# Kernel tuning notes

Measured on AMD Instinct MI355X. Metric: run time of the kernel, lower is better.

Reference implementation:

```python
import jax, jax.numpy as jnp
import numpy as np

B, D = 65536, 784          # batch, input features
H = 256                     # delegator feature (hidden) dim
L = 64                      # num_leaves (experts)
C = 10                      # num_classes


def setup_inputs() -> dict:
    key = jax.random.key(0)
    ks = jax.random.split(key, 7)
    s_in = 1.0 / np.sqrt(D)
    s_h = 1.0 / np.sqrt(H)
    return {
        "x": jax.random.normal(ks[0], (B, D), dtype=jnp.float32),
        "Wf": jax.random.normal(ks[1], (D, H), dtype=jnp.float32) * s_in,   # Node feature proj
        "bf": jnp.zeros((H,), dtype=jnp.float32),
        "Wr": jax.random.normal(ks[2], (D, L), dtype=jnp.float32) * s_in,   # Node router proj
        "br": jnp.zeros((L,), dtype=jnp.float32),
        "Wl": jax.random.normal(ks[3], (L, H, C), dtype=jnp.float32) * s_h,  # per-leaf linear
        "bl": jnp.zeros((L, C), dtype=jnp.float32),
    }


def reference(x, Wf, bf, Wr, br, Wl, bl):
    # Delegator (Node): features + routing probabilities
    features = jax.nn.relu(x @ Wf + bf)                 # [B, H]
    probs = jax.nn.softmax(x @ Wr + br, axis=1)         # [B, L]
    choices = jnp.argmax(probs, axis=1)                 # [B] top-1 leaf per sample
    # Per-sample leaf dispatch: gather each sample's leaf weights, then a
    # batched vec-mat product (memory-bound gather, low FLOP/byte).
    Wc = Wl[choices]                                    # [B, H, C]
    bc = bl[choices]                                    # [B, C]
    predictions = jnp.einsum("bh,bhc->bc", features, Wc) + bc  # [B, C]
    return predictions
```

## Files before the change

### kernel.cpp

```cpp
#include <hip/hip_runtime.h>
#include <stdint.h>

#define B_ROWS 65536
#define D_IN   784
#define H_DIM  256
#define L_LEAF 64
#define C_CLS  10
#define NSTEP2 25
#define BTILE2 20480
#define GAP_THRESH 0.03f

using f32x4    = __attribute__((ext_vector_type(4))) float;
using bf16x8   = __attribute__((ext_vector_type(8))) short;
using ushort8v = __attribute__((ext_vector_type(8))) unsigned short;
using ushort4v = __attribute__((ext_vector_type(4))) unsigned short;

#define O_FLAGCNT  0
#define O_CHOICES  4096
#define O_FLAGROWS (O_CHOICES + B_ROWS * 4)
#define O_WT       (O_FLAGROWS + B_ROWS * 4)
#define WT_BYTES   (NSTEP2 * BTILE2)
#define O_FEAT     (O_WT + WT_BYTES)
#define O_WLB      (O_FEAT + (size_t)B_ROWS * H_DIM * 2)
#define WS_BASE    O_WLB
#define WS_FULL    (O_WLB + (size_t)L_LEAF * H_DIM * C_CLS * 2)

__device__ __forceinline__ unsigned short f2bf(float f) {
    union { float f; unsigned int u; } c; c.f = f;
    unsigned int u = c.u;
    return (unsigned short)((u + 0x7fffu + ((u >> 16) & 1u)) >> 16);
}
__device__ __forceinline__ float bf2f(unsigned short u) {
    union { unsigned int u; float f; } c; c.u = ((unsigned int)u) << 16;
    return c.f;
}
__device__ __forceinline__ unsigned int cvtpk(float a, float b) {
    unsigned int r;
    asm("v_cvt_pk_bf16_f32 %0, %1, %2" : "=v"(r) : "v"(a), "v"(b));
    return r;
}

__device__ __forceinline__ void gload_lds16(const void* g, void* l) {
    __builtin_amdgcn_global_load_lds(
        (const __attribute__((address_space(1))) unsigned int*)g,
        (__attribute__((address_space(3))) unsigned int*)l, 16, 0, 0);
}

__global__ void k0_prep(const float* __restrict__ Wf, const float* __restrict__ Wr,
                        unsigned short* __restrict__ Wt, unsigned int* __restrict__ flagcnt) {
    if (blockIdx.x == 0 && threadIdx.x == 0) *flagcnt = 0u;
    int id = blockIdx.x * 256 + threadIdx.x;
    int ts = id / 1280;
    int r  = id % 1280;
    int n  = r % 320;
    int c  = r / 320;
    int dst = ts * BTILE2 + ((n * 64 + c * 16) ^ ((n & 7) << 4));
    int ks  = ts * 32 + c * 8;
    unsigned short v[8];
    #pragma unroll
    for (int j = 0; j < 8; ++j) {
        int k = ks + j;
        float f = 0.f;
        if (k < D_IN)
            f = (n < H_DIM) ? Wf[(size_t)k * H_DIM + n]
                            : Wr[(size_t)k * L_LEAF + (n - H_DIM)];
        v[j] = f2bf(f);
    }
    *(ushort8v*)((char*)Wt + dst) = *(ushort8v*)v;
}

__global__ void k0b_wl(const float* __restrict__ Wl, unsigned short* __restrict__ Wlb) {
    int i = (blockIdx.x * 256 + threadIdx.x) * 4;
    f32x4 v = *(const f32x4*)(Wl + i);
    ushort4v h; h.x = f2bf(v.x); h.y = f2bf(v.y); h.z = f2bf(v.z); h.w = f2bf(v.w);
    *(ushort4v*)(Wlb + i) = h;
}

__global__ __launch_bounds__(256, 4) void k1_gemm(
    const float* __restrict__ x, const unsigned short* __restrict__ Wt,
    const float* __restrict__ bfv, const float* __restrict__ brv,
    unsigned short* __restrict__ feat, int* __restrict__ choices,
    unsigned int* __restrict__ flagcnt, int* __restrict__ flagrows)
{
    __shared__ __align__(16) unsigned short Bl[2][320 * 32];

    const int t = threadIdx.x, w = t >> 6, l = t & 63, q = l >> 4, ic = l & 15;
    const int bm0 = blockIdx.x * 64;
    const float* xbase = x + (size_t)(bm0 + ic) * D_IN;

    f32x4 acc[4][5];
    #pragma unroll
    for (int a = 0; a < 4; ++a)
        #pragma unroll
        for (int b = 0; b < 5; ++b)
            acc[a][b] = (f32x4){0.f, 0.f, 0.f, 0.f};

    const int rbB = (ic * 64 + (q << 4)) ^ ((ic & 7) << 4);
    const int ntb = w * 5;

    #pragma unroll
    for (int i = 0; i < 5; ++i) {
        int cid = i * 256 + t;
        gload_lds16((const char*)Wt + cid * 16, (char*)&Bl[0][0] + cid * 16);
    }
    __syncthreads();

    int cur = 0;
    for (int ts = 0; ts < NSTEP2; ++ts) {
        if (ts + 1 < NSTEP2) {
            const char* src = (const char*)Wt + (size_t)(ts + 1) * BTILE2;
            char* dst = (char*)&Bl[cur ^ 1][0];
            #pragma unroll
            for (int i = 0; i < 5; ++i) {
                int cid = i * 256 + t;
                gload_lds16(src + cid * 16, dst + cid * 16);
            }
        }
        const int kg = ts * 32 + q * 8;
        const bool ok = (kg + 8 <= D_IN);
        const int kgs = ok ? kg : 0;
        f32x4 an[4][2];
        #pragma unroll
        for (int mt = 0; mt < 4; ++mt) {
            const float* xr = xbase + (size_t)(mt * 16) * D_IN + kgs;
            an[mt][0] = *(const f32x4*)(xr);
            an[mt][1] = *(const f32x4*)(xr + 4);
        }
        bf16x8 af[4];
        #pragma unroll
        for (int mt = 0; mt < 4; ++mt) {
            union { unsigned int u[4]; bf16x8 v; } pk;
            f32x4 lo = an[mt][0], hi = an[mt][1];
            pk.u[0] = ok ? cvtpk(lo.x, lo.y) : 0u;
            pk.u[1] = ok ? cvtpk(lo.z, lo.w) : 0u;
            pk.u[2] = ok ? cvtpk(hi.x, hi.y) : 0u;
            pk.u[3] = ok ? cvtpk(hi.z, hi.w) : 0u;
            af[mt] = pk.v;
        }
        const char* Bc = (const char*)&Bl[cur][0];
        #pragma unroll
        for (int j = 0; j < 5; ++j) {
            bf16x8 b = *(const bf16x8*)(Bc + (ntb + j) * 1024 + rbB);
            #pragma unroll
            for (int mt = 0; mt < 4; ++mt)
                acc[mt][j] = __builtin_amdgcn_mfma_f32_16x16x32_bf16(af[mt], b, acc[mt][j], 0, 0, 0);
        }
        __syncthreads();
        cur ^= 1;
    }

    #pragma unroll
    for (int j = 0; j < 5; ++j) {
        int col = (ntb + j) * 16 + ic;
        if (col < H_DIM) {
            float bias = bfv[col];
            #pragma unroll
            for (int mt = 0; mt < 4; ++mt) {
                #pragma unroll
                for (int i = 0; i < 4; ++i) {
                    int row = bm0 + mt * 16 + q * 4 + i;
                    float v = acc[mt][j][i] + bias;
                    v = v > 0.f ? v : 0.f;
                    feat[(size_t)row * H_DIM + col] = f2bf(v);
                }
            }
        }
    }
    if (w == 3) {
        #pragma unroll
        for (int mt = 0; mt < 4; ++mt) {
            #pragma unroll
            for (int i = 0; i < 4; ++i) {
                float m1 = -1e30f, m2 = -1e30f;
                int a1 = 0;
                #pragma unroll
                for (int j = 1; j < 5; ++j) {
                    int leaf = (j - 1) * 16 + ic;
                    float v = acc[mt][j][i] + brv[leaf];
                    if (v > m1) { m2 = m1; m1 = v; a1 = leaf; }
                    else if (v > m2) { m2 = v; }
                }
                #pragma unroll
                for (int s = 1; s < 16; s <<= 1) {
                    float om1 = __shfl_xor(m1, s, 64);
                    float om2 = __shfl_xor(m2, s, 64);
                    int   oa1 = __shfl_xor(a1, s, 64);
                    bool take = (om1 > m1) || (om1 == m1 && oa1 < a1);
                    float nm2 = take ? fmaxf(om2, m1) : fmaxf(m2, om1);
                    m1 = take ? om1 : m1;
                    a1 = take ? oa1 : a1;
                    m2 = nm2;
                }
                if (ic == 0) {
                    int row = bm0 + mt * 16 + q * 4 + i;
                    choices[row] = a1;
                    if (m1 - m2 < GAP_THRESH) {
                        unsigned int idx = atomicAdd(flagcnt, 1u);
                        flagrows[idx] = row;
                    }
                }
            }
        }
    }
}

__global__ __launch_bounds__(256) void k2_exact(
    const float* __restrict__ x, const float* __restrict__ Wr,
    const float* __restrict__ brv, const unsigned int* __restrict__ flagcnt,
    const int* __restrict__ flagrows, int* __restrict__ choices)
{
    __shared__ float wl[64 * 64];
    __shared__ float xl[4][64];
    const unsigned int cnt = *flagcnt;
    const int t = threadIdx.x, w = t >> 6, l = t & 63;
    for (unsigned int base = blockIdx.x * 4u; base < cnt; base += gridDim.x * 4u) {
        unsigned int ri = base + w;
        int row = (ri < cnt) ? flagrows[ri] : 0;
        const float* xr = x + (size_t)row * D_IN;
        float s0 = 0.f, s1 = 0.f, s2 = 0.f, s3 = 0.f;
        for (int kt = 0; kt < 13; ++kt) {
            int k0 = kt * 64;
            #pragma unroll
            for (int i = 0; i < 4; ++i) {
                int flat = i * 256 + t;
                int kk = flat >> 4, lq = (flat & 15) * 4;
                int kgk = k0 + kk;
                f32x4 v = (f32x4){0.f, 0.f, 0.f, 0.f};
                if (kgk < D_IN) v = *(const f32x4*)(Wr + (size_t)kgk * L_LEAF + lq);
                *(f32x4*)&wl[kk * 64 + lq] = v;
            }
            xl[w][l] = (k0 + l < D_IN) ? xr[k0 + l] : 0.f;
            __syncthreads();
            #pragma unroll
            for (int kk = 0; kk < 64; kk += 4) {
                s0 = fmaf(xl[w][kk    ], wl[(kk    ) * 64 + l], s0);
                s1 = fmaf(xl[w][kk + 1], wl[(kk + 1) * 64 + l], s1);
                s2 = fmaf(xl[w][kk + 2], wl[(kk + 2) * 64 + l], s2);
                s3 = fmaf(xl[w][kk + 3], wl[(kk + 3) * 64 + l], s3);
            }
            __syncthreads();
        }
        float v = (s0 + s1) + (s2 + s3) + brv[l];
        int a = l;
        #pragma unroll
        for (int st = 1; st < 64; st <<= 1) {
            float ov = __shfl_xor(v, st, 64);
            int   oa = __shfl_xor(a, st, 64);
            if (ov > v || (ov == v && oa < a)) { v = ov; a = oa; }
        }
        if (l == 0 && ri < cnt) choices[row] = a;
    }
}

__global__ __launch_bounds__(256) void k3_leaf(
    const unsigned short* __restrict__ feat, const int* __restrict__ choices,
    const float* __restrict__ Wl, const unsigned short* __restrict__ Wlb,
    const float* __restrict__ blv, float* __restrict__ out)
{
    const int t = threadIdx.x, wv = t >> 6, l = t & 63, g = l >> 4, i = l & 15;
    const int row = blockIdx.x * 16 + wv * 4 + g;
    const int leaf = choices[row];

    ushort8v f0 = *(const ushort8v*)(feat + (size_t)row * H_DIM + i * 16);
    ushort8v f1 = *(const ushort8v*)(feat + (size_t)row * H_DIM + i * 16 + 8);
    float fv[16];
    #pragma unroll
    for (int j = 0; j < 8; ++j) { fv[j] = bf2f(f0[j]); fv[8 + j] = bf2f(f1[j]); }

    float acc[C_CLS];
    #pragma unroll
    for (int c = 0; c < C_CLS; ++c) acc[c] = 0.f;

    if (Wlb) {
        const unsigned short* wp = Wlb + ((size_t)leaf * H_DIM + i * 16) * C_CLS;
        ushort8v wreg[20];
        #pragma unroll
        for (int j = 0; j < 20; ++j) wreg[j] = *(const ushort8v*)(wp + j * 8);
        #pragma unroll
        for (int h = 0; h < 16; ++h) {
            #pragma unroll
            for (int c = 0; c < C_CLS; ++c) {
                int e = h * C_CLS + c;
                acc[c] = fmaf(fv[h], bf2f(wreg[e >> 3][e & 7]), acc[c]);
            }
        }
    } else {
        const float* wp = Wl + ((size_t)leaf * H_DIM + i * 16) * C_CLS;
        #pragma unroll
        for (int h = 0; h < 16; ++h) {
            #pragma unroll
            for (int c = 0; c < C_CLS; ++c)
                acc[c] = fmaf(fv[h], wp[h * C_CLS + c], acc[c]);
        }
    }
    #pragma unroll
    for (int st = 1; st < 16; st <<= 1) {
        #pragma unroll
        for (int c = 0; c < C_CLS; ++c) acc[c] += __shfl_xor(acc[c], st, 64);
    }
    if (i == 0) {
        #pragma unroll
        for (int c = 0; c < C_CLS; ++c)
            out[(size_t)row * C_CLS + c] = acc[c] + blv[leaf * C_CLS + c];
    }
}

extern "C" void kernel_launch(void* const* d_in, const int* in_sizes, int n_in,
                              void* d_out, int out_size, void* d_ws, size_t ws_size,
                              hipStream_t stream) {
    if (ws_size < WS_BASE) return;
    const bool use_bf = ws_size >= WS_FULL;

    const float* x   = (const float*)d_in[0];
    const float* Wf  = (const float*)d_in[1];
    const float* bfv = (const float*)d_in[2];
    const float* Wr  = (const float*)d_in[3];
    const float* brv = (const float*)d_in[4];
    const float* Wl  = (const float*)d_in[5];
    const float* blv = (const float*)d_in[6];
    float* out = (float*)d_out;

    char* ws = (char*)d_ws;
    unsigned int*   flagcnt  = (unsigned int*)(ws + O_FLAGCNT);
    int*            choices  = (int*)(ws + O_CHOICES);
    int*            flagrows = (int*)(ws + O_FLAGROWS);
    unsigned short* Wt       = (unsigned short*)(ws + O_WT);
    unsigned short* feat     = (unsigned short*)(ws + O_FEAT);
    unsigned short* Wlb      = use_bf ? (unsigned short*)(ws + O_WLB) : (unsigned short*)0;

    hipLaunchKernelGGL(k0_prep, dim3(125), dim3(256), 0, stream, Wf, Wr, Wt, flagcnt);
    if (use_bf)
        hipLaunchKernelGGL(k0b_wl, dim3(160), dim3(256), 0, stream, Wl, Wlb);
    hipLaunchKernelGGL(k1_gemm, dim3(B_ROWS / 64), dim3(256), 0, stream,
                       x, Wt, bfv, brv, feat, choices, flagcnt, flagrows);
    hipLaunchKernelGGL(k2_exact, dim3(1024), dim3(256), 0, stream,
                       x, Wr, brv, flagcnt, flagrows, choices);
    hipLaunchKernelGGL(k3_leaf, dim3(B_ROWS / 16), dim3(256), 0, stream,
                       feat, choices, Wl, Wlb, blv, out);
}
```

Measured before the change: 211.7 us.

## Pre-convert x to swizzled bf16 tiles and stage both operands via LDS

Adds a pre-pass that converts x to bf16 in a tiled, XOR-swizzled layout in workspace, then the GEMM loads both A and B tiles into LDS via global_load_lds with K-step 64 (13 steps). This removes per-thread strided fp32 loads and in-loop conversion from the GEMM. In exchange it adds an extra full pass writing and re-reading a ~100MB bf16 copy of x, and drops the double-buffered prefetch so loads are no longer overlapped with MFMA. The old path is kept as a fallback when workspace is too small.

New measurement: 244.1 us. 15.3% more time.

```diff
diff --git a/kernel.cpp b/kernel.cpp
--- a/kernel.cpp
+++ b/kernel.cpp
@@ -6,6 +6,8 @@
 #define H_DIM  256
 #define L_LEAF 64
 #define C_CLS  10
+#define NSTEP  13
+#define BTILE  40960
 #define NSTEP2 25
 #define BTILE2 20480
 #define GAP_THRESH 0.03f
@@ -19,11 +21,15 @@
 #define O_CHOICES  4096
 #define O_FLAGROWS (O_CHOICES + B_ROWS * 4)
 #define O_WT       (O_FLAGROWS + B_ROWS * 4)
-#define WT_BYTES   (NSTEP2 * BTILE2)
-#define O_FEAT     (O_WT + WT_BYTES)
+#define WT_MAX     532480
+#define O_FEAT     (O_WT + WT_MAX)
 #define O_WLB      (O_FEAT + (size_t)B_ROWS * H_DIM * 2)
+#define WLB_BYTES  ((size_t)L_LEAF * H_DIM * C_CLS * 2)
+#define O_XT       (O_WLB + WLB_BYTES)
+#define XT_BYTES   ((size_t)(B_ROWS / 64) * NSTEP * 8192)
 #define WS_BASE    O_WLB
-#define WS_FULL    (O_WLB + (size_t)L_LEAF * H_DIM * C_CLS * 2)
+#define WS_WLB     (O_WLB + WLB_BYTES)
+#define WS_XT      (O_XT + XT_BYTES)
 
 __device__ __forceinline__ unsigned short f2bf(float f) {
     union { float f; unsigned int u; } c; c.f = f;
@@ -39,23 +45,23 @@
     asm("v_cvt_pk_bf16_f32 %0, %1, %2" : "=v"(r) : "v"(a), "v"(b));
     return r;
 }
-
 __device__ __forceinline__ void gload_lds16(const void* g, void* l) {
     __builtin_amdgcn_global_load_lds(
         (const __attribute__((address_space(1))) unsigned int*)g,
         (__attribute__((address_space(3))) unsigned int*)l, 16, 0, 0);
 }
 
-__global__ void k0_prep(const float* __restrict__ Wf, const float* __restrict__ Wr,
-                        unsigned short* __restrict__ Wt, unsigned int* __restrict__ flagcnt) {
+
+__global__ void k0_prep64(const float* __restrict__ Wf, const float* __restrict__ Wr,
+                          unsigned short* __restrict__ Wt, unsigned int* __restrict__ flagcnt) {
     if (blockIdx.x == 0 && threadIdx.x == 0) *flagcnt = 0u;
     int id = blockIdx.x * 256 + threadIdx.x;
-    int ts = id / 1280;
-    int r  = id % 1280;
+    if (id >= 33280) return;
+    int ts = id / 2560;
+    int r  = id % 2560;
     int n  = r % 320;
-    int c  = r / 320;
-    int dst = ts * BTILE2 + ((n * 64 + c * 16) ^ ((n & 7) << 4));
-    int ks  = ts * 32 + c * 8;
+    int c4 = r / 320;
+    int ks = ts * 64 + ((c4 ^ (n & 7)) << 3);
     unsigned short v[8];
     #pragma unroll
     for (int j = 0; j < 8; ++j) {
@@ -66,7 +72,25 @@
                             : Wr[(size_t)k * L_LEAF + (n - H_DIM)];
         v[j] = f2bf(f);
     }
-    *(ushort8v*)((char*)Wt + dst) = *(ushort8v*)v;
+    *(ushort8v*)((char*)Wt + (size_t)ts * BTILE + (size_t)(n * 8 + c4) * 16) = *(ushort8v*)v;
+}
+
+__global__ void k0x(const float* __restrict__ x, unsigned short* __restrict__ Xt) {
+    int id = blockIdx.x * 256 + threadIdx.x;
+    int row = id / 104, c = id % 104;
+    int ts = c >> 3, cc = c & 7;
+    int bm = row >> 6, rr = row & 63, mt = rr >> 4, ic = rr & 15;
+    size_t dst = ((size_t)(bm * NSTEP + ts) * 4 + mt) * 2048
+               + (size_t)(ic * 128 + ((cc ^ (ic & 7)) << 4));
+    ushort8v v = (ushort8v){0,0,0,0,0,0,0,0};
+    if (c < 98) {
+        const float* xp = x + (size_t)row * D_IN + c * 8;
+        f32x4 lo = *(const f32x4*)(xp);
+        f32x4 hi = *(const f32x4*)(xp + 4);
+        v.s0 = f2bf(lo.x); v.s1 = f2bf(lo.y); v.s2 = f2bf(lo.z); v.s3 = f2bf(lo.w);
+        v.s4 = f2bf(hi.x); v.s5 = f2bf(hi.y); v.s6 = f2bf(hi.z); v.s7 = f2bf(hi.w);
+    }
+    *(ushort8v*)((char*)Xt + dst) = v;
 }
 
 __global__ void k0b_wl(const float* __restrict__ Wl, unsigned short* __restrict__ Wlb) {
@@ -76,17 +100,16 @@
     *(ushort4v*)(Wlb + i) = h;
 }
 
-__global__ __launch_bounds__(256, 4) void k1_gemm(
-    const float* __restrict__ x, const unsigned short* __restrict__ Wt,
+__global__ __launch_bounds__(256, 3) void k1_xt(
+    const unsigned short* __restrict__ Xt, const unsigned short* __restrict__ Wt,
     const float* __restrict__ bfv, const float* __restrict__ brv,
     unsigned short* __restrict__ feat, int* __restrict__ choices,
     unsigned int* __restrict__ flagcnt, int* __restrict__ flagrows)
 {
-    __shared__ __align__(16) unsigned short Bl[2][320 * 32];
+    __shared__ __align__(16) char L[49152];
 
     const int t = threadIdx.x, w = t >> 6, l = t & 63, q = l >> 4, ic = l & 15;
     const int bm0 = blockIdx.x * 64;
-    const float* xbase = x + (size_t)(bm0 + ic) * D_IN;
 
     f32x4 acc[4][5];
     #pragma unroll
@@ -95,58 +118,43 @@
         for (int b = 0; b < 5; ++b)
             acc[a][b] = (f32x4){0.f, 0.f, 0.f, 0.f};
 
-    const int rbB = (ic * 64 + (q << 4)) ^ ((ic & 7) << 4);
-    const int ntb = w * 5;
-
-    #pragma unroll
-    for (int i = 0; i < 5; ++i) {
-        int cid = i * 256 + t;
-        gload_lds16((const char*)Wt + cid * 16, (char*)&Bl[0][0] + cid * 16);
-    }
-    __syncthreads();
-
-    int cur = 0;
-    for (int ts = 0; ts < NSTEP2; ++ts) {
-        if (ts + 1 < NSTEP2) {
-            const char* src = (const char*)Wt + (size_t)(ts + 1) * BTILE2;
-            char* dst = (char*)&Bl[cur ^ 1][0];
-            #pragma unroll
-            for (int i = 0; i < 5; ++i) {
-                int cid = i * 256 + t;
-                gload_lds16(src + cid * 16, dst + cid * 16);
-            }
-        }
-        const int kg = ts * 32 + q * 8;
-        const bool ok = (kg + 8 <= D_IN);
-        const int kgs = ok ? kg : 0;
-        f32x4 an[4][2];
+    const int e7   = ic & 7;
+    const int p0   = ((q ^ e7) << 4);
+    const int p1   = (((4 + q) ^ e7) << 4);
+    const int arow = ic * 128;
+    const int ntb  = w * 5;
+
+    for (int ts = 0; ts < NSTEP; ++ts) {
+        const char* asrc = (const char*)Xt + (size_t)(blockIdx.x * NSTEP + ts) * 8192;
+        gload_lds16(asrc + t * 16,          L + t * 16);
+        gload_lds16(asrc + (256 + t) * 16,  L + (256 + t) * 16);
+        const char* bsrc = (const char*)Wt + (size_t)ts * BTILE;
+        #pragma unroll
+        for (int i = 0; i < 10; ++i) {
+            int cid = i * 256 + t;
+            gload_lds16(bsrc + cid * 16, L + 8192 + cid * 16);
+        }
+        __syncthreads();
+
+        bf16x8 a0[4], a1[4];
         #pragma unroll
         for (int mt = 0; mt < 4; ++mt) {
-            const float* xr = xbase + (size_t)(mt * 16) * D_IN + kgs;
-            an[mt][0] = *(const f32x4*)(xr);
-            an[mt][1] = *(const f32x4*)(xr + 4);
-        }
-        bf16x8 af[4];
-        #pragma unroll
-        for (int mt = 0; mt < 4; ++mt) {
-            union { unsigned int u[4]; bf16x8 v; } pk;
-            f32x4 lo = an[mt][0], hi = an[mt][1];
-            pk.u[0] = ok ? cvtpk(lo.x, lo.y) : 0u;
-            pk.u[1] = ok ? cvtpk(lo.z, lo.w) : 0u;
-            pk.u[2] = ok ? cvtpk(hi.x, hi.y) : 0u;
-            pk.u[3] = ok ? cvtpk(hi.z, hi.w) : 0u;
-            af[mt] = pk.v;
-        }
-        const char* Bc = (const char*)&Bl[cur][0];
+            a0[mt] = *(const bf16x8*)(L + mt * 2048 + arow + p0);
+            a1[mt] = *(const bf16x8*)(L + mt * 2048 + arow + p1);
+        }
         #pragma unroll
         for (int j = 0; j < 5; ++j) {
-            bf16x8 b = *(const bf16x8*)(Bc + (ntb + j) * 1024 + rbB);
+            const char* bs = L + 8192 + (ntb + j) * 2048 + arow;
+            bf16x8 b0 = *(const bf16x8*)(bs + p0);
             #pragma unroll
             for (int mt = 0; mt < 4; ++mt)
-                acc[mt][j] = __builtin_amdgcn_mfma_f32_16x16x32_bf16(af[mt], b, acc[mt][j], 0, 0, 0);
+                acc[mt][j] = __builtin_amdgcn_mfma_f32_16x16x32_bf16(a0[mt], b0, acc[mt][j], 0, 0, 0);
+            bf16x8 b1 = *(const bf16x8*)(bs + p1);
+            #pragma unroll
+            for (int mt = 0; mt < 4; ++mt)
+                acc[mt][j] = __builtin_amdgcn_mfma_f32_16x16x32_bf16(a1[mt], b1, acc[mt][j], 0, 0, 0);
         }
         __syncthreads();
-        cur ^= 1;
     }
 
     #pragma unroll
@@ -203,6 +211,153 @@
         }
     }
 }
+
+
+__global__ void k0_prep32(const float* __restrict__ Wf, const float* __restrict__ Wr,
+                          unsigned short* __restrict__ Wt, unsigned int* __restrict__ flagcnt) {
+    if (blockIdx.x == 0 && threadIdx.x == 0) *flagcnt = 0u;
+    int id = blockIdx.x * 256 + threadIdx.x;
+    int ts = id / 1280;
+    int r  = id % 1280;
+    int n  = r % 320;
+    int c  = r / 320;
+    int dst = ts * BTILE2 + ((n * 64 + c * 16) ^ ((n & 7) << 4));
+    int ks  = ts * 32 + c * 8;
+    unsigned short v[8];
+    #pragma unroll
+    for (int j = 0; j < 8; ++j) {
+        int k = ks + j;
+        float f = 0.f;
+        if (k < D_IN)
+            f = (n < H_DIM) ? Wf[(size_t)k * H_DIM + n]
+                            : Wr[(size_t)k * L_LEAF + (n - H_DIM)];
+        v[j] = f2bf(f);
+    }
+    *(ushort8v*)((char*)Wt + dst) = *(ushort8v*)v;
+}
+
+__global__ __launch_bounds__(256, 4) void k1_direct(
+    const float* __restrict__ x, const unsigned short* __restrict__ Wt,
+    const float* __restrict__ bfv, const float* __restrict__ brv,
+    unsigned short* __restrict__ feat, int* __restrict__ choices,
+    unsigned int* __restrict__ flagcnt, int* __restrict__ flagrows)
+{
+    __shared__ __align__(16) unsigned short Bl[2][320 * 32];
+    const int t = threadIdx.x, w = t >> 6, l = t & 63, q = l >> 4, ic = l & 15;
+    const int bm0 = blockIdx.x * 64;
+    const float* xbase = x + (size_t)(bm0 + ic) * D_IN;
+    f32x4 acc[4][5];
+    #pragma unroll
+    for (int a = 0; a < 4; ++a)
+        #pragma unroll
+        for (int b = 0; b < 5; ++b)
+            acc[a][b] = (f32x4){0.f, 0.f, 0.f, 0.f};
+    const int rbB = (ic * 64 + (q << 4)) ^ ((ic & 7) << 4);
+    const int ntb = w * 5;
+    #pragma unroll
+    for (int i = 0; i < 5; ++i) {
+        int cid = i * 256 + t;
+        gload_lds16((const char*)Wt + cid * 16, (char*)&Bl[0][0] + cid * 16);
+    }
+    __syncthreads();
+    int cur = 0;
+    for (int ts = 0; ts < NSTEP2; ++ts) {
+        if (ts + 1 < NSTEP2) {
+            const char* src = (const char*)Wt + (size_t)(ts + 1) * BTILE2;
+            char* dst = (char*)&Bl[cur ^ 1][0];
+            #pragma unroll
+            for (int i = 0; i < 5; ++i) {
+                int cid = i * 256 + t;
+                gload_lds16(src + cid * 16, dst + cid * 16);
+            }
+        }
+        const int kg = ts * 32 + q * 8;
+        const bool ok = (kg + 8 <= D_IN);
+        const int kgs = ok ? kg : 0;
+        f32x4 an[4][2];
+        #pragma unroll
+        for (int mt = 0; mt < 4; ++mt) {
+            const float* xr = xbase + (size_t)(mt * 16) * D_IN + kgs;
+            an[mt][0] = *(const f32x4*)(xr);
+            an[mt][1] = *(const f32x4*)(xr + 4);
+        }
+        bf16x8 af[4];
+        #pragma unroll
+        for (int mt = 0; mt < 4; ++mt) {
+            union { unsigned int u[4]; bf16x8 v; } pk;
+            f32x4 lo = an[mt][0], hi = an[mt][1];
+            pk.u[0] = ok ? cvtpk(lo.x, lo.y) : 0u;
+            pk.u[1] = ok ? cvtpk(lo.z, lo.w) : 0u;
+            pk.u[2] = ok ? cvtpk(hi.x, hi.y) : 0u;
+            pk.u[3] = ok ? cvtpk(hi.z, hi.w) : 0u;
+            af[mt] = pk.v;
+        }
+        const char* Bc = (const char*)&Bl[cur][0];
+        #pragma unroll
+        for (int j = 0; j < 5; ++j) {
+            bf16x8 b = *(const bf16x8*)(Bc + (ntb + j) * 1024 + rbB);
+            #pragma unroll
+            for (int mt = 0; mt < 4; ++mt)
+                acc[mt][j] = __builtin_amdgcn_mfma_f32_16x16x32_bf16(af[mt], b, acc[mt][j], 0, 0, 0);
+        }
+        __syncthreads();
+        cur ^= 1;
+    }
+    #pragma unroll
+    for (int j = 0; j < 5; ++j) {
+        int col = (ntb + j) * 16 + ic;
+        if (col < H_DIM) {
+            float bias = bfv[col];
+            #pragma unroll
+            for (int mt = 0; mt < 4; ++mt) {
+                #pragma unroll
+                for (int i = 0; i < 4; ++i) {
+                    int row = bm0 + mt * 16 + q * 4 + i;
+                    float v = acc[mt][j][i] + bias;
+                    v = v > 0.f ? v : 0.f;
+                    feat[(size_t)row * H_DIM + col] = f2bf(v);
+                }
+            }
+        }
+    }
+    if (w == 3) {
+        #pragma unroll
+        for (int mt = 0; mt < 4; ++mt) {
+            #pragma unroll
+            for (int i = 0; i < 4; ++i) {
+                float m1 = -1e30f, m2 = -1e30f;
+                int a1 = 0;
+                #pragma unroll
+                for (int j = 1; j < 5; ++j) {
+                    int leaf = (j - 1) * 16 + ic;
+                    float v = acc[mt][j][i] + brv[leaf];
+                    if (v > m1) { m2 = m1; m1 = v; a1 = leaf; }
+                    else if (v > m2) { m2 = v; }
+                }
+                #pragma unroll
+                for (int s = 1; s < 16; s <<= 1) {
+                    float om1 = __shfl_xor(m1, s, 64);
+                    float om2 = __shfl_xor(m2, s, 64);
+                    int   oa1 = __shfl_xor(a1, s, 64);
+                    bool take = (om1 > m1) || (om1 == m1 && oa1 < a1);
+                    float nm2 = take ? fmaxf(om2, m1) : fmaxf(m2, om1);
+                    m1 = take ? om1 : m1;
+                    a1 = take ? oa1 : a1;
+                    m2 = nm2;
+                }
+                if (ic == 0) {
+                    int row = bm0 + mt * 16 + q * 4 + i;
+                    choices[row] = a1;
+                    if (m1 - m2 < GAP_THRESH) {
+                        unsigned int idx = atomicAdd(flagcnt, 1u);
+                        flagrows[idx] = row;
+                    }
+                }
+            }
+        }
+    }
+}
+
 
 __global__ __launch_bounds__(256) void k2_exact(
     const float* __restrict__ x, const float* __restrict__ Wr,
@@ -309,7 +464,8 @@
                               void* d_out, int out_size, void* d_ws, size_t ws_size,
                               hipStream_t stream) {
     if (ws_size < WS_BASE) return;
-    const bool use_bf = ws_size >= WS_FULL;
+    const bool use_bf = ws_size >= WS_WLB;
+    const bool use_xt = ws_size >= WS_XT;
 
     const float* x   = (const float*)d_in[0];
     const float* Wf  = (const float*)d_in[1];
@@ -327,12 +483,21 @@
     unsigned short* Wt       = (unsigned short*)(ws + O_WT);
     unsigned short* feat     = (unsigned short*)(ws + O_FEAT);
     unsigned short* Wlb      = use_bf ? (unsigned short*)(ws + O_WLB) : (unsigned short*)0;
-
-    hipLaunchKernelGGL(k0_prep, dim3(125), dim3(256), 0, stream, Wf, Wr, Wt, flagcnt);
+    unsigned short* Xt       = (unsigned short*)(ws + O_XT);
+
     if (use_bf)
         hipLaunchKernelGGL(k0b_wl, dim3(160), dim3(256), 0, stream, Wl, Wlb);
-    hipLaunchKernelGGL(k1_gemm, dim3(B_ROWS / 64), dim3(256), 0, stream,
-                       x, Wt, bfv, brv, feat, choices, flagcnt, flagrows);
+
+    if (use_xt) {
+        hipLaunchKernelGGL(k0_prep64, dim3(130), dim3(256), 0, stream, Wf, Wr, Wt, flagcnt);
+        hipLaunchKernelGGL(k0x, dim3(26624), dim3(256), 0, stream, x, Xt);
+        hipLaunchKernelGGL(k1_xt, dim3(B_ROWS / 64), dim3(256), 0, stream,
+                           Xt, Wt, bfv, brv, feat, choices, flagcnt, flagrows);
+    } else {
+        hipLaunchKernelGGL(k0_prep32, dim3(125), dim3(256), 0, stream, Wf, Wr, Wt, flagcnt);
+        hipLaunchKernelGGL(k1_direct, dim3(B_ROWS / 64), dim3(256), 0, stream,
+                           x, Wt, bfv, brv, feat, choices, flagcnt, flagrows);
+    }
     hipLaunchKernelGGL(k2_exact, dim3(1024), dim3(256), 0, stream,
                        x, Wr, brv, flagcnt, flagrows, choices);
     hipLaunchKernelGGL(k3_leaf, dim3(B_ROWS / 16), dim3(256), 0, stream,
```

## Triple-buffer x and weight tiles in LDS with async global-to-LDS loads

Applied to the files above, without the earlier changes.

The feature/router GEMM now uses 128-row tiles with 512 threads per block. Both the fp32 x tile and the bf16 weight tile are staged into a three-deep LDS ring with global_load_lds, two steps ahead, instead of loading x straight from global into registers each step. A manual vmcnt wait plus barrier replaces __syncthreads, and s_setprio is raised around the MFMA block. The aim is to hide x load latency behind compute and to share weight tiles across twice as many rows. In exchange, about 108 KB of LDS limits each CU to one block, and the K tail reads duplicate x values that are cancelled only by the zero-padded weights.

New measurement: 198.9 us. 1.06x faster.

```diff
diff --git a/kernel.cpp b/kernel.cpp
--- a/kernel.cpp
+++ b/kernel.cpp
@@ -19,11 +19,11 @@
 #define O_CHOICES  4096
 #define O_FLAGROWS (O_CHOICES + B_ROWS * 4)
 #define O_WT       (O_FLAGROWS + B_ROWS * 4)
-#define WT_BYTES   (NSTEP2 * BTILE2)
-#define O_FEAT     (O_WT + WT_BYTES)
+#define O_FEAT     (O_WT + NSTEP2 * BTILE2)
 #define O_WLB      (O_FEAT + (size_t)B_ROWS * H_DIM * 2)
+#define WLB_BYTES  ((size_t)L_LEAF * H_DIM * C_CLS * 2)
 #define WS_BASE    O_WLB
-#define WS_FULL    (O_WLB + (size_t)L_LEAF * H_DIM * C_CLS * 2)
+#define WS_WLB     (O_WLB + WLB_BYTES)
 
 __device__ __forceinline__ unsigned short f2bf(float f) {
     union { float f; unsigned int u; } c; c.f = f;
@@ -39,15 +39,14 @@
     asm("v_cvt_pk_bf16_f32 %0, %1, %2" : "=v"(r) : "v"(a), "v"(b));
     return r;
 }
-
 __device__ __forceinline__ void gload_lds16(const void* g, void* l) {
     __builtin_amdgcn_global_load_lds(
         (const __attribute__((address_space(1))) unsigned int*)g,
         (__attribute__((address_space(3))) unsigned int*)l, 16, 0, 0);
 }
 
-__global__ void k0_prep(const float* __restrict__ Wf, const float* __restrict__ Wr,
-                        unsigned short* __restrict__ Wt, unsigned int* __restrict__ flagcnt) {
+__global__ void k0_prep32(const float* __restrict__ Wf, const float* __restrict__ Wr,
+                          unsigned short* __restrict__ Wt, unsigned int* __restrict__ flagcnt) {
     if (blockIdx.x == 0 && threadIdx.x == 0) *flagcnt = 0u;
     int id = blockIdx.x * 256 + threadIdx.x;
     int ts = id / 1280;
@@ -76,17 +75,20 @@
     *(ushort4v*)(Wlb + i) = h;
 }
 
-__global__ __launch_bounds__(256, 4) void k1_gemm(
+#define BUFB 36864
+__global__ __launch_bounds__(512, 1) void k1_pipe(
     const float* __restrict__ x, const unsigned short* __restrict__ Wt,
     const float* __restrict__ bfv, const float* __restrict__ brv,
     unsigned short* __restrict__ feat, int* __restrict__ choices,
     unsigned int* __restrict__ flagcnt, int* __restrict__ flagrows)
 {
-    __shared__ __align__(16) unsigned short Bl[2][320 * 32];
-
-    const int t = threadIdx.x, w = t >> 6, l = t & 63, q = l >> 4, ic = l & 15;
-    const int bm0 = blockIdx.x * 64;
-    const float* xbase = x + (size_t)(bm0 + ic) * D_IN;
+    __shared__ __align__(16) char L[3 * BUFB];
+
+    const int t  = threadIdx.x;
+    const int w  = t >> 6, l = t & 63, q = l >> 4, ic = l & 15;
+    const int wm = w >> 2, wn = w & 3;
+    const int bm0 = blockIdx.x * 128;
+    const int ntb = wn * 5;
 
     f32x4 acc[4][5];
     #pragma unroll
@@ -95,59 +97,72 @@
         for (int b = 0; b < 5; ++b)
             acc[a][b] = (f32x4){0.f, 0.f, 0.f, 0.f};
 
-    const int rbB = (ic * 64 + (q << 4)) ^ ((ic & 7) << 4);
-    const int ntb = w * 5;
-
-    #pragma unroll
-    for (int i = 0; i < 5; ++i) {
-        int cid = i * 256 + t;
-        gload_lds16((const char*)Wt + cid * 16, (char*)&Bl[0][0] + cid * 16);
-    }
-    __syncthreads();
-
-    int cur = 0;
+    const int e7  = ic & 7;
+    const int pA0 = ((2 * q)     ^ e7) << 4;
+    const int pA1 = ((2 * q + 1) ^ e7) << 4;
+    const int rbB = (ic * 64 + (q << 4)) ^ (e7 << 4);
+
+#define STAGE(TS, LB)                                                          \
+    {                                                                          \
+        const int ts_ = (TS);                                                  \
+        char* Lb_ = (LB);                                                      \
+        _Pragma("unroll")                                                      \
+        for (int h = 0; h < 2; ++h) {                                          \
+            int i_ = h * 512 + t;                                              \
+            int r_ = i_ >> 3, p_ = i_ & 7;                                     \
+            int c8_ = p_ ^ (r_ & 7);                                           \
+            int k_ = ts_ * 32 + c8_ * 4;                                       \
+            int ko_ = (k_ + 4 <= D_IN) ? k_ : 0;                               \
+            gload_lds16(x + (size_t)(bm0 + r_) * D_IN + ko_, Lb_ + i_ * 16);   \
+        }                                                                      \
+        const char* bs_ = (const char*)Wt + (size_t)ts_ * BTILE2;              \
+        char* bd_ = Lb_ + 16384;                                               \
+        gload_lds16(bs_ + t * 16,          bd_ + t * 16);                      \
+        gload_lds16(bs_ + (512 + t) * 16,  bd_ + (512 + t) * 16);              \
+        if (t < 256)                                                           \
+            gload_lds16(bs_ + (1024 + t) * 16, bd_ + (1024 + t) * 16);         \
+    }
+
+    STAGE(0, L);
+    STAGE(1, L + BUFB);
+
     for (int ts = 0; ts < NSTEP2; ++ts) {
-        if (ts + 1 < NSTEP2) {
-            const char* src = (const char*)Wt + (size_t)(ts + 1) * BTILE2;
-            char* dst = (char*)&Bl[cur ^ 1][0];
-            #pragma unroll
-            for (int i = 0; i < 5; ++i) {
-                int cid = i * 256 + t;
-                gload_lds16(src + cid * 16, dst + cid * 16);
-            }
-        }
-        const int kg = ts * 32 + q * 8;
-        const bool ok = (kg + 8 <= D_IN);
-        const int kgs = ok ? kg : 0;
-        f32x4 an[4][2];
+        if (ts < NSTEP2 - 1)
+            asm volatile("s_waitcnt vmcnt(4)\ns_barrier" ::: "memory");
+        else
+            asm volatile("s_waitcnt vmcnt(0)\ns_barrier" ::: "memory");
+
+        if (ts + 2 < NSTEP2) {
+            char* nb = L + ((ts + 2) % 3) * BUFB;
+            STAGE(ts + 2, nb);
+        }
+
+        const char* Lc = L + (ts % 3) * BUFB;
+        bf16x8 af[4];
         #pragma unroll
         for (int mt = 0; mt < 4; ++mt) {
-            const float* xr = xbase + (size_t)(mt * 16) * D_IN + kgs;
-            an[mt][0] = *(const f32x4*)(xr);
-            an[mt][1] = *(const f32x4*)(xr + 4);
-        }
-        bf16x8 af[4];
-        #pragma unroll
-        for (int mt = 0; mt < 4; ++mt) {
+            const char* rowp = Lc + (wm * 64 + mt * 16 + ic) * 128;
+            f32x4 lo = *(const f32x4*)(rowp + pA0);
+            f32x4 hi = *(const f32x4*)(rowp + pA1);
             union { unsigned int u[4]; bf16x8 v; } pk;
-            f32x4 lo = an[mt][0], hi = an[mt][1];
-            pk.u[0] = ok ? cvtpk(lo.x, lo.y) : 0u;
-            pk.u[1] = ok ? cvtpk(lo.z, lo.w) : 0u;
-            pk.u[2] = ok ? cvtpk(hi.x, hi.y) : 0u;
-            pk.u[3] = ok ? cvtpk(hi.z, hi.w) : 0u;
+            pk.u[0] = cvtpk(lo.x, lo.y);
+            pk.u[1] = cvtpk(lo.z, lo.w);
+            pk.u[2] = cvtpk(hi.x, hi.y);
+            pk.u[3] = cvtpk(hi.z, hi.w);
             af[mt] = pk.v;
         }
-        const char* Bc = (const char*)&Bl[cur][0];
+        const char* Bb = Lc + 16384;
+        __builtin_amdgcn_s_setprio(1);
         #pragma unroll
         for (int j = 0; j < 5; ++j) {
-            bf16x8 b = *(const bf16x8*)(Bc + (ntb + j) * 1024 + rbB);
+            bf16x8 b = *(const bf16x8*)(Bb + (ntb + j) * 1024 + rbB);
             #pragma unroll
             for (int mt = 0; mt < 4; ++mt)
                 acc[mt][j] = __builtin_amdgcn_mfma_f32_16x16x32_bf16(af[mt], b, acc[mt][j], 0, 0, 0);
         }
-        __syncthreads();
-        cur ^= 1;
-    }
+        __builtin_amdgcn_s_setprio(0);
+    }
+#undef STAGE
 
     #pragma unroll
     for (int j = 0; j < 5; ++j) {
@@ -158,7 +173,7 @@
             for (int mt = 0; mt < 4; ++mt) {
                 #pragma unroll
                 for (int i = 0; i < 4; ++i) {
-                    int row = bm0 + mt * 16 + q * 4 + i;
+                    int row = bm0 + wm * 64 + mt * 16 + q * 4 + i;
                     float v = acc[mt][j][i] + bias;
                     v = v > 0.f ? v : 0.f;
                     feat[(size_t)row * H_DIM + col] = f2bf(v);
@@ -166,7 +181,7 @@
             }
         }
     }
-    if (w == 3) {
+    if (wn == 3) {
         #pragma unroll
         for (int mt = 0; mt < 4; ++mt) {
             #pragma unroll
@@ -192,7 +207,7 @@
                     m2 = nm2;
                 }
                 if (ic == 0) {
-                    int row = bm0 + mt * 16 + q * 4 + i;
+                    int row = bm0 + wm * 64 + mt * 16 + q * 4 + i;
                     choices[row] = a1;
                     if (m1 - m2 < GAP_THRESH) {
                         unsigned int idx = atomicAdd(flagcnt, 1u);
@@ -309,7 +324,7 @@
                               void* d_out, int out_size, void* d_ws, size_t ws_size,
                               hipStream_t stream) {
     if (ws_size < WS_BASE) return;
-    const bool use_bf = ws_size >= WS_FULL;
+    const bool use_bf = ws_size >= WS_WLB;
 
     const float* x   = (const float*)d_in[0];
     const float* Wf  = (const float*)d_in[1];
@@ -328,10 +343,10 @@
     unsigned short* feat     = (unsigned short*)(ws + O_FEAT);
     unsigned short* Wlb      = use_bf ? (unsigned short*)(ws + O_WLB) : (unsigned short*)0;
 
-    hipLaunchKernelGGL(k0_prep, dim3(125), dim3(256), 0, stream, Wf, Wr, Wt, flagcnt);
+    hipLaunchKernelGGL(k0_prep32, dim3(125), dim3(256), 0, stream, Wf, Wr, Wt, flagcnt);
     if (use_bf)
         hipLaunchKernelGGL(k0b_wl, dim3(160), dim3(256), 0, stream, Wl, Wlb);
-    hipLaunchKernelGGL(k1_gemm, dim3(B_ROWS / 64), dim3(256), 0, stream,
+    hipLaunchKernelGGL(k1_pipe, dim3(B_ROWS / 128), dim3(512), 0, stream,
                        x, Wt, bfv, brv, feat, choices, flagcnt, flagrows);
     hipLaunchKernelGGL(k2_exact, dim3(1024), dim3(256), 0, stream,
                        x, Wr, brv, flagcnt, flagrows, choices);
```

## Stage whole x row-panel in LDS as bf16 before the main GEMM loop

Applied to the files above, without the earlier changes.

The GEMM kernel now loads the block's full 64x784 x panel from global memory up front, converts it to bf16 and stores it in LDS with a padded stride. The K-loop then reads A fragments from LDS instead of issuing strided global loads every step. Blocks grow to 512 threads (8 waves, 2x4 wave grid), each wave holding half the accumulators, and s_setprio is raised around the MFMA bursts. The change uses about 140KB of LDS, so only one block fits per CU, and the upfront panel load is not overlapped with compute, which risks latency exposure.

New measurement: 210.9 us. No clear change (-0.4%).

```diff
diff --git a/kernel.cpp b/kernel.cpp
--- a/kernel.cpp
+++ b/kernel.cpp
@@ -14,16 +14,21 @@
 using bf16x8   = __attribute__((ext_vector_type(8))) short;
 using ushort8v = __attribute__((ext_vector_type(8))) unsigned short;
 using ushort4v = __attribute__((ext_vector_type(4))) unsigned short;
+using uintx2   = __attribute__((ext_vector_type(2))) unsigned int;
 
 #define O_FLAGCNT  0
 #define O_CHOICES  4096
 #define O_FLAGROWS (O_CHOICES + B_ROWS * 4)
 #define O_WT       (O_FLAGROWS + B_ROWS * 4)
-#define WT_BYTES   (NSTEP2 * BTILE2)
-#define O_FEAT     (O_WT + WT_BYTES)
+#define O_FEAT     (O_WT + NSTEP2 * BTILE2)
 #define O_WLB      (O_FEAT + (size_t)B_ROWS * H_DIM * 2)
+#define WLB_BYTES  ((size_t)L_LEAF * H_DIM * C_CLS * 2)
 #define WS_BASE    O_WLB
-#define WS_FULL    (O_WLB + (size_t)L_LEAF * H_DIM * C_CLS * 2)
+#define WS_WLB     (O_WLB + WLB_BYTES)
+
+#define PSTRIDE    1576
+#define PANEL_PAD  102448
+#define LDS_TOTAL  (PANEL_PAD + 2 * BTILE2)
 
 __device__ __forceinline__ unsigned short f2bf(float f) {
     union { float f; unsigned int u; } c; c.f = f;
@@ -39,15 +44,14 @@
     asm("v_cvt_pk_bf16_f32 %0, %1, %2" : "=v"(r) : "v"(a), "v"(b));
     return r;
 }
-
 __device__ __forceinline__ void gload_lds16(const void* g, void* l) {
     __builtin_amdgcn_global_load_lds(
         (const __attribute__((address_space(1))) unsigned int*)g,
         (__attribute__((address_space(3))) unsigned int*)l, 16, 0, 0);
 }
 
-__global__ void k0_prep(const float* __restrict__ Wf, const float* __restrict__ Wr,
-                        unsigned short* __restrict__ Wt, unsigned int* __restrict__ flagcnt) {
+__global__ void k0_prep32(const float* __restrict__ Wf, const float* __restrict__ Wr,
+                          unsigned short* __restrict__ Wt, unsigned int* __restrict__ flagcnt) {
     if (blockIdx.x == 0 && threadIdx.x == 0) *flagcnt = 0u;
     int id = blockIdx.x * 256 + threadIdx.x;
     int ts = id / 1280;
@@ -76,75 +80,80 @@
     *(ushort4v*)(Wlb + i) = h;
 }
 
-__global__ __launch_bounds__(256, 4) void k1_gemm(
+__global__ __launch_bounds__(512, 1) void k1_panel(
     const float* __restrict__ x, const unsigned short* __restrict__ Wt,
     const float* __restrict__ bfv, const float* __restrict__ brv,
     unsigned short* __restrict__ feat, int* __restrict__ choices,
     unsigned int* __restrict__ flagcnt, int* __restrict__ flagrows)
 {
-    __shared__ __align__(16) unsigned short Bl[2][320 * 32];
+    __shared__ __align__(16) char L[LDS_TOTAL];
 
     const int t = threadIdx.x, w = t >> 6, l = t & 63, q = l >> 4, ic = l & 15;
+    const int wm = w >> 2, wn = w & 3;
     const int bm0 = blockIdx.x * 64;
-    const float* xbase = x + (size_t)(bm0 + ic) * D_IN;
-
-    f32x4 acc[4][5];
-    #pragma unroll
-    for (int a = 0; a < 4; ++a)
+    const int ntb = wn * 5;
+    const int e7  = ic & 7;
+    const int rbB = (ic * 64 + (q << 4)) ^ (e7 << 4);
+
+    {
+        const char* bs = (const char*)Wt;
+        char* bd = L + PANEL_PAD;
+        gload_lds16(bs + t * 16,          bd + t * 16);
+        gload_lds16(bs + (512 + t) * 16,  bd + (512 + t) * 16);
+        if (t < 256)
+            gload_lds16(bs + (1024 + t) * 16, bd + (1024 + t) * 16);
+    }
+    const float* xp = x + (size_t)bm0 * D_IN;
+    #pragma unroll 5
+    for (int rd = 0; rd < 25; ++rd) {
+        int flat = rd * 512 + t;
+        if (flat < 12544) {
+            f32x4 v = *(const f32x4*)(xp + (size_t)flat * 4);
+            int row  = flat / 196;
+            int koff = flat - row * 196;
+            uintx2 p;
+            p.x = cvtpk(v.x, v.y);
+            p.y = cvtpk(v.z, v.w);
+            *(uintx2*)(L + row * PSTRIDE + koff * 8) = p;
+        }
+    }
+    __syncthreads();
+
+    f32x4 acc[2][5];
+    #pragma unroll
+    for (int a = 0; a < 2; ++a)
         #pragma unroll
         for (int b = 0; b < 5; ++b)
             acc[a][b] = (f32x4){0.f, 0.f, 0.f, 0.f};
-
-    const int rbB = (ic * 64 + (q << 4)) ^ ((ic & 7) << 4);
-    const int ntb = w * 5;
-
-    #pragma unroll
-    for (int i = 0; i < 5; ++i) {
-        int cid = i * 256 + t;
-        gload_lds16((const char*)Wt + cid * 16, (char*)&Bl[0][0] + cid * 16);
-    }
-    __syncthreads();
 
     int cur = 0;
     for (int ts = 0; ts < NSTEP2; ++ts) {
         if (ts + 1 < NSTEP2) {
-            const char* src = (const char*)Wt + (size_t)(ts + 1) * BTILE2;
-            char* dst = (char*)&Bl[cur ^ 1][0];
-            #pragma unroll
-            for (int i = 0; i < 5; ++i) {
-                int cid = i * 256 + t;
-                gload_lds16(src + cid * 16, dst + cid * 16);
-            }
+            const char* bs = (const char*)Wt + (size_t)(ts + 1) * BTILE2;
+            char* bd = L + PANEL_PAD + (cur ^ 1) * BTILE2;
+            gload_lds16(bs + t * 16,          bd + t * 16);
+            gload_lds16(bs + (512 + t) * 16,  bd + (512 + t) * 16);
+            if (t < 256)
+                gload_lds16(bs + (1024 + t) * 16, bd + (1024 + t) * 16);
         }
         const int kg = ts * 32 + q * 8;
         const bool ok = (kg + 8 <= D_IN);
-        const int kgs = ok ? kg : 0;
-        f32x4 an[4][2];
-        #pragma unroll
-        for (int mt = 0; mt < 4; ++mt) {
-            const float* xr = xbase + (size_t)(mt * 16) * D_IN + kgs;
-            an[mt][0] = *(const f32x4*)(xr);
-            an[mt][1] = *(const f32x4*)(xr + 4);
-        }
-        bf16x8 af[4];
-        #pragma unroll
-        for (int mt = 0; mt < 4; ++mt) {
-            union { unsigned int u[4]; bf16x8 v; } pk;
-            f32x4 lo = an[mt][0], hi = an[mt][1];
-            pk.u[0] = ok ? cvtpk(lo.x, lo.y) : 0u;
-            pk.u[1] = ok ? cvtpk(lo.z, lo.w) : 0u;
-            pk.u[2] = ok ? cvtpk(hi.x, hi.y) : 0u;
-            pk.u[3] = ok ? cvtpk(hi.z, hi.w) : 0u;
-            af[mt] = pk.v;
-        }
-        const char* Bc = (const char*)&Bl[cur][0];
+        bf16x8 af[2];
+        #pragma unroll
+        for (int mt = 0; mt < 2; ++mt) {
+            bf16x8 v = *(const bf16x8*)(L + (wm * 32 + mt * 16 + ic) * PSTRIDE
+                                          + ts * 64 + q * 16);
+            af[mt] = ok ? v : (bf16x8){0,0,0,0,0,0,0,0};
+        }
+        const char* Bb = L + PANEL_PAD + cur * BTILE2;
+        __builtin_amdgcn_s_setprio(1);
         #pragma unroll
         for (int j = 0; j < 5; ++j) {
-            bf16x8 b = *(const bf16x8*)(Bc + (ntb + j) * 1024 + rbB);
-            #pragma unroll
-            for (int mt = 0; mt < 4; ++mt)
-                acc[mt][j] = __builtin_amdgcn_mfma_f32_16x16x32_bf16(af[mt], b, acc[mt][j], 0, 0, 0);
-        }
+            bf16x8 b = *(const bf16x8*)(Bb + (ntb + j) * 1024 + rbB);
+            acc[0][j] = __builtin_amdgcn_mfma_f32_16x16x32_bf16(af[0], b, acc[0][j], 0, 0, 0);
+            acc[1][j] = __builtin_amdgcn_mfma_f32_16x16x32_bf16(af[1], b, acc[1][j], 0, 0, 0);
+        }
+        __builtin_amdgcn_s_setprio(0);
         __syncthreads();
         cur ^= 1;
     }
@@ -155,10 +164,10 @@
         if (col < H_DIM) {
             float bias = bfv[col];
             #pragma unroll
-            for (int mt = 0; mt < 4; ++mt) {
+            for (int mt = 0; mt < 2; ++mt) {
                 #pragma unroll
                 for (int i = 0; i < 4; ++i) {
-                    int row = bm0 + mt * 16 + q * 4 + i;
+                    int row = bm0 + wm * 32 + mt * 16 + q * 4 + i;
                     float v = acc[mt][j][i] + bias;
                     v = v > 0.f ? v : 0.f;
                     feat[(size_t)row * H_DIM + col] = f2bf(v);
@@ -166,9 +175,9 @@
             }
         }
     }
-    if (w == 3) {
-        #pragma unroll
-        for (int mt = 0; mt < 4; ++mt) {
+    if (wn == 3) {
+        #pragma unroll
+        for (int mt = 0; mt < 2; ++mt) {
             #pragma unroll
             for (int i = 0; i < 4; ++i) {
                 float m1 = -1e30f, m2 = -1e30f;
@@ -192,7 +201,7 @@
                     m2 = nm2;
                 }
                 if (ic == 0) {
-                    int row = bm0 + mt * 16 + q * 4 + i;
+                    int row = bm0 + wm * 32 + mt * 16 + q * 4 + i;
                     choices[row] = a1;
                     if (m1 - m2 < GAP_THRESH) {
                         unsigned int idx = atomicAdd(flagcnt, 1u);
@@ -309,7 +318,7 @@
                               void* d_out, int out_size, void* d_ws, size_t ws_size,
                               hipStream_t stream) {
     if (ws_size < WS_BASE) return;
-    const bool use_bf = ws_size >= WS_FULL;
+    const bool use_bf = ws_size >= WS_WLB;
 
     const float* x   = (const float*)d_in[0];
     const float* Wf  = (const float*)d_in[1];
@@ -328,10 +337,10 @@
     unsigned short* feat     = (unsigned short*)(ws + O_FEAT);
     unsigned short* Wlb      = use_bf ? (unsigned short*)(ws + O_WLB) : (unsigned short*)0;
 
-    hipLaunchKernelGGL(k0_prep, dim3(125), dim3(256), 0, stream, Wf, Wr, Wt, flagcnt);
+    hipLaunchKernelGGL(k0_prep32, dim3(125), dim3(256), 0, stream, Wf, Wr, Wt, flagcnt);
     if (use_bf)
         hipLaunchKernelGGL(k0b_wl, dim3(160), dim3(256), 0, stream, Wl, Wlb);
-    hipLaunchKernelGGL(k1_gemm, dim3(B_ROWS / 64), dim3(256), 0, stream,
+    hipLaunchKernelGGL(k1_panel, dim3(B_ROWS / 64), dim3(512), 0, stream,
                        x, Wt, bfv, brv, feat, choices, flagcnt, flagrows);
     hipLaunchKernelGGL(k2_exact, dim3(1024), dim3(256), 0, stream,
                        x, Wr, brv, flagcnt, flagrows, choices);
```
